# Performance work log

Measured on AMD Instinct MI355X. Metric: run time of the kernel, lower is better.

## Reference

```python
import jax, jax.numpy as jnp
import numpy as np

B, N, C, H = 4, 2048, 768, 12
D = C // H  # head_dim = 64

def setup_inputs() -> dict:
    key = jax.random.key(0)
    ks = jax.random.split(key, 6)
    s = 0.02
    return {
        "img_tokens": jax.random.normal(ks[0], (B, N, C), jnp.float32),
        "ln_gamma": jnp.ones((C,), jnp.float32),
        "ln_beta": jnp.zeros((C,), jnp.float32),
        "w_qkv": jax.random.normal(ks[1], (C, 3 * C), jnp.float32) * s,
        "w_out": jax.random.normal(ks[2], (C, C), jnp.float32) * s,
        "b_out": jnp.zeros((C,), jnp.float32),
    }

def reference(img_tokens, ln_gamma, ln_beta, w_qkv, w_out, b_out):
    x = img_tokens
    # LayerNorm over channel dim
    mu = jnp.mean(x, axis=-1, keepdims=True)
    var = jnp.var(x, axis=-1, keepdims=True)
    xn = (x - mu) * jax.lax.rsqrt(var + 1e-5) * ln_gamma + ln_beta
    qkv = xn @ w_qkv                      # [B, N, 3C]
    q, k, v = jnp.split(qkv, 3, axis=-1)
    def heads(t):                          # [B, N, C] -> [B, H, N, D]
        return t.reshape(B, N, H, D).transpose(0, 2, 1, 3)
    q, k, v = heads(q), heads(k), heads(v)
    scale = 1.0 / np.sqrt(D).astype(np.float32)
    scores = jnp.einsum('bhnd,bhmd->bhnm', q, k) * scale  # [B, H, N, N]
    attn = jax.nn.softmax(scores, axis=-1)
    out = jnp.einsum('bhnm,bhmd->bhnd', attn, v)          # [B, H, N, D]
    out = out.transpose(0, 2, 1, 3).reshape(B, N, C)
    out = out @ w_out + b_out
    return out + img_tokens
```

## Files before the change

### kernel.cpp

```cpp
#include <hip/hip_runtime.h>


typedef __bf16 bf16x8 __attribute__((ext_vector_type(8)));
typedef float  f32x4  __attribute__((ext_vector_type(4)));
typedef unsigned int u32x4 __attribute__((ext_vector_type(4)));

#define MFMA16(a,b,c) __builtin_amdgcn_mfma_f32_16x16x32_bf16((a),(b),(c),0,0,0)

__device__ inline f32x4 zero4() { f32x4 z = {0.f,0.f,0.f,0.f}; return z; }

__device__ inline void gll16(const __bf16* g, __bf16* l) {
  __builtin_amdgcn_global_load_lds((const __attribute__((address_space(1))) unsigned int*)g,
                                   (__attribute__((address_space(3))) unsigned int*)l,
                                   16, 0, 0);
}

__device__ inline unsigned cvt_pk_bf16(float lo, float hi) {
  unsigned r;
  asm("v_cvt_pk_bf16_f32 %0, %1, %2" : "=v"(r) : "v"(lo), "v"(hi));
  return r;
}
__device__ inline void permlane32_swap(unsigned &a, unsigned &b) {
  asm("v_permlane32_swap_b32 %0, %1" : "+v"(a), "+v"(b));
}
__device__ inline void permlane16_swap(unsigned &a, unsigned &b) {
  asm("v_permlane16_swap_b32 %0, %1" : "+v"(a), "+v"(b));
}

__global__ __launch_bounds__(256) void ln_kernel(const float* __restrict__ x,
                                                 const float* __restrict__ g,
                                                 const float* __restrict__ bt,
                                                 __bf16* __restrict__ xn) {
  const int row = blockIdx.x;
  const int tid = threadIdx.x;
  const float* xr = x + (size_t)row * 768;
  float v[3]; float s = 0.f, ss = 0.f;
  #pragma unroll
  for (int i = 0; i < 3; ++i) { float f = xr[tid + 256*i]; v[i] = f; s += f; ss += f*f; }
  #pragma unroll
  for (int m = 32; m >= 1; m >>= 1) { s += __shfl_xor(s, m, 64); ss += __shfl_xor(ss, m, 64); }
  __shared__ float red[8];
  const int wave = tid >> 6;
  if ((tid & 63) == 0) { red[wave] = s; red[4 + wave] = ss; }
  __syncthreads();
  s  = red[0] + red[1] + red[2] + red[3];
  ss = red[4] + red[5] + red[6] + red[7];
  const float mu  = s * (1.f/768.f);
  const float var = ss * (1.f/768.f) - mu*mu;
  const float inv = rsqrtf(var + 1e-5f);
  __bf16* xo = xn + (size_t)row * 768;
  #pragma unroll
  for (int i = 0; i < 3; ++i) {
    const int c0 = tid + 256*i;
    xo[c0] = (__bf16)((v[i] - mu) * inv * g[c0] + bt[c0]);
  }
}

__global__ __launch_bounds__(256) void transpose_kernel(const float* __restrict__ in,
                                                        __bf16* __restrict__ out,
                                                        int R, int C) {
  __shared__ float t[32][33];
  const int tx = threadIdx.x & 31, ty = threadIdx.x >> 5;
  const int c0 = blockIdx.x * 32, r0 = blockIdx.y * 32;
  #pragma unroll
  for (int p = 0; p < 4; ++p) t[ty + 8*p][tx] = in[(size_t)(r0 + ty + 8*p) * C + c0 + tx];
  __syncthreads();
  #pragma unroll
  for (int p = 0; p < 4; ++p) out[(size_t)(c0 + ty + 8*p) * R + r0 + tx] = (__bf16)t[tx][ty + 8*p];
}

template<int KDIM>
__device__ inline void gemm_mainloop(const __bf16* __restrict__ A, const __bf16* __restrict__ BT,
                                     int bm, int bn, int wave, int lane,
                                     f32x4 acc[4][4], __bf16* Asm, __bf16* Bsm) {
  const int wm = wave >> 1, wn = wave & 1;
  const int lr = lane & 15, lk = lane >> 4;
  for (int k0 = 0; k0 < KDIM; k0 += 64) {
    #pragma unroll
    for (int s2 = 0; s2 < 4; ++s2) {
      const int st = wave * 4 + s2;
      const int rb = st >> 1, kh = st & 1;
      gll16(A  + (size_t)(bm + rb*16 + lr) * KDIM + k0 + kh*32 + lk*8, Asm + st*512);
      gll16(BT + (size_t)(bn + rb*16 + lr) * KDIM + k0 + kh*32 + lk*8, Bsm + st*512);
    }
    __builtin_amdgcn_s_waitcnt(0);
    __syncthreads();
    #pragma unroll
    for (int ks = 0; ks < 2; ++ks) {
      bf16x8 a[4], b[4];
      #pragma unroll
      for (int mt = 0; mt < 4; ++mt) a[mt] = *(const bf16x8*)(Asm + ((wm*4+mt)*2+ks)*512 + lane*8);
      #pragma unroll
      for (int nt = 0; nt < 4; ++nt) b[nt] = *(const bf16x8*)(Bsm + ((wn*4+nt)*2+ks)*512 + lane*8);
      #pragma unroll
      for (int mt = 0; mt < 4; ++mt)
        #pragma unroll
        for (int nt = 0; nt < 4; ++nt)
          acc[mt][nt] = MFMA16(a[mt], b[nt], acc[mt][nt]);
    }
    __syncthreads();
  }
}

__global__ __launch_bounds__(256) void gemm_qkv_kernel(const __bf16* __restrict__ A,
                                                       const __bf16* __restrict__ BT,
                                                       __bf16* __restrict__ q,
                                                       __bf16* __restrict__ k,
                                                       __bf16* __restrict__ vt) {
  __shared__ __align__(16) __bf16 smem[2*8192];
  __bf16* Asm = smem;
  __bf16* Bsm = smem + 8192;
  const int lane = threadIdx.x & 63, wave = threadIdx.x >> 6;
  const int bm = blockIdx.y * 128, bn = blockIdx.x * 128;
  f32x4 acc[4][4];
  #pragma unroll
  for (int i = 0; i < 4; ++i)
    #pragma unroll
    for (int j = 0; j < 4; ++j) acc[i][j] = zero4();
  gemm_mainloop<768>(A, BT, bm, bn, wave, lane, acc, Asm, Bsm);
  const int wm = wave >> 1, wn = wave & 1;
  const int quad = lane >> 4, c = lane & 15;
  if (bn < 1536) {
    const float qscale = 0.125f * 1.44269504088896f;
    #pragma unroll
    for (int mt = 0; mt < 4; ++mt)
      #pragma unroll
      for (int nt = 0; nt < 4; ++nt) {
        const int col = bn + wn*64 + nt*16 + c;
        const int which = col >= 768 ? 1 : 0;
        const int within = col - which*768;
        const int h = within >> 6, d = within & 63;
        #pragma unroll
        for (int r = 0; r < 4; ++r) {
          const int row = bm + wm*64 + mt*16 + quad*4 + r;
          const int b = row >> 11, n = row & 2047;
          const float vv = acc[mt][nt][r];
          const size_t idx = ((size_t)(b*12 + h) * 2048 + n) * 64 + d;
          if (which == 0) q[idx] = (__bf16)(vv * qscale);
          else            k[idx] = (__bf16)vv;
        }
      }
  } else {
    __syncthreads();
    #pragma unroll
    for (int mt = 0; mt < 4; ++mt)
      #pragma unroll
      for (int nt = 0; nt < 4; ++nt) {
        const int lcol = wn*64 + nt*16 + c;
        #pragma unroll
        for (int r = 0; r < 4; ++r) {
          const int lrow = wm*64 + mt*16 + quad*4 + r;
          smem[lrow*66 + lcol] = (__bf16)acc[mt][nt][r];
        }
      }
    __syncthreads();
    const int b = bm >> 11, n0 = bm & 2047;
    const int vo = bn - 1536;
    const int n = threadIdx.x & 127;
    const int csel = threadIdx.x >> 7;
    #pragma unroll
    for (int pass = 0; pass < 64; ++pass) {
      const int lc = pass*2 + csel;
      const int gcol = vo + lc;
      const int h = gcol >> 6, d = gcol & 63;
      vt[((size_t)(b*12 + h)*64 + d)*2048 + n0 + n] = smem[n*66 + lc];
    }
  }
}

__global__ __launch_bounds__(256) void gemm_out_kernel(const __bf16* __restrict__ A,
                                                       const __bf16* __restrict__ BT,
                                                       const float* __restrict__ bias,
                                                       const float* __restrict__ resid,
                                                       float* __restrict__ out) {
  __shared__ __align__(16) __bf16 Asm[16*512];
  __shared__ __align__(16) __bf16 Bsm[16*512];
  const int lane = threadIdx.x & 63, wave = threadIdx.x >> 6;
  const int bm = blockIdx.y * 128, bn = blockIdx.x * 128;
  f32x4 acc[4][4];
  #pragma unroll
  for (int i = 0; i < 4; ++i)
    #pragma unroll
    for (int j = 0; j < 4; ++j) acc[i][j] = zero4();
  gemm_mainloop<768>(A, BT, bm, bn, wave, lane, acc, Asm, Bsm);
  const int wm = wave >> 1, wn = wave & 1;
  const int quad = lane >> 4, c = lane & 15;
  #pragma unroll
  for (int mt = 0; mt < 4; ++mt)
    #pragma unroll
    for (int nt = 0; nt < 4; ++nt) {
      const int col = bn + wn*64 + nt*16 + c;
      #pragma unroll
      for (int r = 0; r < 4; ++r) {
        const int row = bm + wm*64 + mt*16 + quad*4 + r;
        out[(size_t)row*768 + col] = acc[mt][nt][r] + bias[col] + resid[(size_t)row*768 + col];
      }
    }
}

__global__ __launch_bounds__(512, 6) void attn_kernel(const __bf16* __restrict__ q,
                                                      const __bf16* __restrict__ k,
                                                      const __bf16* __restrict__ vt,
                                                      __bf16* __restrict__ o) {
  const int xcd = blockIdx.x & 7, i = blockIdx.x >> 3;
  const int bh = xcd * 6 + (i >> 4);
  const int qt = i & 15;
  const int lane = threadIdx.x & 63, wave = threadIdx.x >> 6;
  const int c = lane & 15, quad = lane >> 4;
  const int lr = lane & 15, lk = lane >> 4;
  const int q0 = qt*128 + wave*16;

  const __bf16* qb = q  + ((size_t)bh*2048 + q0) * 64;
  const __bf16* kb = k  + (size_t)bh * 2048 * 64;
  const __bf16* vb = vt + (size_t)bh * 64 * 2048;

  __shared__ __align__(16) __bf16 Ksm[2][4096];
  __shared__ __align__(16) __bf16 Vsm[2][4096];

  bf16x8 aq[2];
  aq[0] = *(const bf16x8*)(qb + (size_t)c*64 + quad*8);
  aq[1] = *(const bf16x8*)(qb + (size_t)c*64 + 32 + quad*8);

  float cl = 0.f;
  f32x4 od[4];
  #pragma unroll
  for (int r = 0; r < 4; ++r) od[r] = zero4();

  auto stage = [&](int it) {
    const int kt = it * 64;
    __bf16* Ks = Ksm[it & 1];
    __bf16* Vs = Vsm[it & 1];
    gll16(kb + (size_t)(kt + (wave>>1)*16 + lr) * 64 + (wave&1)*32 + lk*8,  Ks + wave*512);
    gll16(vb + (size_t)((wave>>1)*16 + lr) * 2048 + kt + (wave&1)*32 + lk*8, Vs + wave*512);
  };

  stage(0);
  stage(1);

  for (int it = 0; it < 32; ++it) {
    const __bf16* Ks = Ksm[it & 1];
    const __bf16* Vs = Vsm[it & 1];
    if (it < 31) asm volatile("s_waitcnt vmcnt(2)" ::: "memory");
    else         asm volatile("s_waitcnt vmcnt(0)" ::: "memory");
    asm volatile("s_barrier" ::: "memory");
    #pragma unroll
    for (int ch = 0; ch < 2; ++ch) {
      unsigned pk[2][2];
      #pragma unroll
      for (int t2 = 0; t2 < 2; ++t2) {
        const int t = ch*2 + t2;
        const bf16x8 ka0 = *(const bf16x8*)(Ks + (t*2+0)*512 + lane*8);
        const bf16x8 ka1 = *(const bf16x8*)(Ks + (t*2+1)*512 + lane*8);
        f32x4 z = zero4();
        __builtin_amdgcn_s_setprio(1);
        z = MFMA16(ka0, aq[0], z);
        z = MFMA16(ka1, aq[1], z);
        __builtin_amdgcn_s_setprio(0);
        const float p0 = __builtin_amdgcn_exp2f(z[0]);
        const float p1 = __builtin_amdgcn_exp2f(z[1]);
        const float p2 = __builtin_amdgcn_exp2f(z[2]);
        const float p3 = __builtin_amdgcn_exp2f(z[3]);
        cl += (p0 + p1) + (p2 + p3);
        pk[t2][0] = cvt_pk_bf16(p0, p1);
        pk[t2][1] = cvt_pk_bf16(p2, p3);
      }
      unsigned s0 = pk[0][0], s2 = pk[1][0];
      permlane32_swap(s0, s2);
      permlane16_swap(s0, s2);
      unsigned s1 = pk[0][1], s3 = pk[1][1];
      permlane32_swap(s1, s3);
      permlane16_swap(s1, s3);
      u32x4 w4; w4.x = s0; w4.y = s1; w4.z = s2; w4.w = s3;
      const bf16x8 pa = __builtin_bit_cast(bf16x8, w4);
      __builtin_amdgcn_s_setprio(1);
      #pragma unroll
      for (int dt = 0; dt < 4; ++dt) {
        const bf16x8 bv = *(const bf16x8*)(Vs + (dt*2+ch)*512 + lane*8);
        od[dt] = MFMA16(pa, bv, od[dt]);
      }
      __builtin_amdgcn_s_setprio(0);
    }
    asm volatile("s_barrier" ::: "memory");
    if (it + 2 < 32) stage(it + 2);
  }
  const int b = bh / 12, h = bh % 12;
  float s = cl;
  s += __shfl_xor(s, 16, 64);
  s += __shfl_xor(s, 32, 64);
  float rl[4];
  #pragma unroll
  for (int r = 0; r < 4; ++r) rl[r] = 1.f / __shfl(s, quad*4 + r, 64);
  #pragma unroll
  for (int dt = 0; dt < 4; ++dt)
    #pragma unroll
    for (int r = 0; r < 4; ++r) {
      const int n = q0 + quad*4 + r;
      const int col = h*64 + dt*16 + c;
      o[((size_t)b*2048 + n)*768 + col] = (__bf16)(od[dt][r] * rl[r]);
    }
}

extern "C" void kernel_launch(void* const* d_in, const int* in_sizes, int n_in,
                              void* d_out, int out_size, void* d_ws, size_t ws_size,
                              hipStream_t stream) {
  const float* img   = (const float*)d_in[0];
  const float* gamma = (const float*)d_in[1];
  const float* beta  = (const float*)d_in[2];
  const float* wqkv  = (const float*)d_in[3];
  const float* wout  = (const float*)d_in[4];
  const float* bout  = (const float*)d_in[5];
  float* out = (float*)d_out;

  __bf16* ws = (__bf16*)d_ws;
  size_t off = 0;
  __bf16* xn    = ws + off; off += (size_t)8192*768;
  __bf16* wqkvT = ws + off; off += (size_t)2304*768;
  __bf16* woutT = ws + off; off += (size_t)768*768;
  __bf16* qs    = ws + off; off += (size_t)48*2048*64;
  __bf16* ks    = ws + off; off += (size_t)48*2048*64;
  __bf16* vts   = ws + off; off += (size_t)48*64*2048;
  __bf16* os    = ws + off; off += (size_t)8192*768;

  ln_kernel<<<8192, 256, 0, stream>>>(img, gamma, beta, xn);
  transpose_kernel<<<dim3(72, 24), 256, 0, stream>>>(wqkv, wqkvT, 768, 2304);
  transpose_kernel<<<dim3(24, 24), 256, 0, stream>>>(wout, woutT, 768, 768);
  gemm_qkv_kernel<<<dim3(18, 64), 256, 0, stream>>>(xn, wqkvT, qs, ks, vts);
  attn_kernel<<<768, 512, 0, stream>>>(qs, ks, vts, os);
  gemm_out_kernel<<<dim3(6, 64), 256, 0, stream>>>(os, woutT, bout, img, out);
}
```

Measured before the change: 254.8 us.

## Double-buffer GEMM mainloop LDS tiles with async prefetch two stages ahead

```diff
diff --git a/kernel.cpp b/kernel.cpp
--- a/kernel.cpp
+++ b/kernel.cpp
@@ -75,30 +75,44 @@
                                      f32x4 acc[4][4], __bf16* Asm, __bf16* Bsm) {
   const int wm = wave >> 1, wn = wave & 1;
   const int lr = lane & 15, lk = lane >> 4;
-  for (int k0 = 0; k0 < KDIM; k0 += 64) {
+  constexpr int NIT = KDIM / 64;
+  auto stage = [&](int t) {
+    const int k0 = t * 64;
+    __bf16* Ad = Asm + (t & 1) * 8192;
+    __bf16* Bd = Bsm + (t & 1) * 8192;
     #pragma unroll
     for (int s2 = 0; s2 < 4; ++s2) {
       const int st = wave * 4 + s2;
       const int rb = st >> 1, kh = st & 1;
-      gll16(A  + (size_t)(bm + rb*16 + lr) * KDIM + k0 + kh*32 + lk*8, Asm + st*512);
-      gll16(BT + (size_t)(bn + rb*16 + lr) * KDIM + k0 + kh*32 + lk*8, Bsm + st*512);
-    }
-    __builtin_amdgcn_s_waitcnt(0);
-    __syncthreads();
+      gll16(A  + (size_t)(bm + rb*16 + lr) * KDIM + k0 + kh*32 + lk*8, Ad + st*512);
+      gll16(BT + (size_t)(bn + rb*16 + lr) * KDIM + k0 + kh*32 + lk*8, Bd + st*512);
+    }
+  };
+  stage(0);
+  stage(1);
+  for (int t = 0; t < NIT; ++t) {
+    if (t + 1 < NIT) asm volatile("s_waitcnt vmcnt(8)" ::: "memory");
+    else             asm volatile("s_waitcnt vmcnt(0)" ::: "memory");
+    asm volatile("s_barrier" ::: "memory");
+    const __bf16* Ab = Asm + (t & 1) * 8192;
+    const __bf16* Bb = Bsm + (t & 1) * 8192;
     #pragma unroll
     for (int ks = 0; ks < 2; ++ks) {
       bf16x8 a[4], b[4];
       #pragma unroll
-      for (int mt = 0; mt < 4; ++mt) a[mt] = *(const bf16x8*)(Asm + ((wm*4+mt)*2+ks)*512 + lane*8);
-      #pragma unroll
-      for (int nt = 0; nt < 4; ++nt) b[nt] = *(const bf16x8*)(Bsm + ((wn*4+nt)*2+ks)*512 + lane*8);
+      for (int mt = 0; mt < 4; ++mt) a[mt] = *(const bf16x8*)(Ab + ((wm*4+mt)*2+ks)*512 + lane*8);
+      #pragma unroll
+      for (int nt = 0; nt < 4; ++nt) b[nt] = *(const bf16x8*)(Bb + ((wn*4+nt)*2+ks)*512 + lane*8);
+      __builtin_amdgcn_s_setprio(1);
       #pragma unroll
       for (int mt = 0; mt < 4; ++mt)
         #pragma unroll
         for (int nt = 0; nt < 4; ++nt)
           acc[mt][nt] = MFMA16(a[mt], b[nt], acc[mt][nt]);
-    }
-    __syncthreads();
+      __builtin_amdgcn_s_setprio(0);
+    }
+    asm volatile("s_barrier" ::: "memory");
+    if (t + 2 < NIT) stage(t + 2);
   }
 }
 
@@ -107,9 +121,9 @@
                                                        __bf16* __restrict__ q,
                                                        __bf16* __restrict__ k,
                                                        __bf16* __restrict__ vt) {
-  __shared__ __align__(16) __bf16 smem[2*8192];
+  __shared__ __align__(16) __bf16 smem[4*8192];
   __bf16* Asm = smem;
-  __bf16* Bsm = smem + 8192;
+  __bf16* Bsm = smem + 2*8192;
   const int lane = threadIdx.x & 63, wave = threadIdx.x >> 6;
   const int bm = blockIdx.y * 128, bn = blockIdx.x * 128;
   f32x4 acc[4][4];
@@ -173,8 +187,8 @@
                                                        const float* __restrict__ bias,
                                                        const float* __restrict__ resid,
                                                        float* __restrict__ out) {
-  __shared__ __align__(16) __bf16 Asm[16*512];
-  __shared__ __align__(16) __bf16 Bsm[16*512];
+  __shared__ __align__(16) __bf16 Asm[2*8192];
+  __shared__ __align__(16) __bf16 Bsm[2*8192];
   const int lane = threadIdx.x & 63, wave = threadIdx.x >> 6;
   const int bm = blockIdx.y * 128, bn = blockIdx.x * 128;
   f32x4 acc[4][4];
```

After: 246.9 us. 3.1% less time.
